# Performance work log

Hardware: AMD Instinct MI355X
Metric: run time of the kernel (lower is better)

The kernel has to match this reference:

```python
import jax, jax.numpy as jnp
import numpy as np

B, L, H = 2, 2048, 1024
NH, HD = 16, 64  # n_heads, head_size


def setup_inputs() -> dict:
    key = jax.random.key(0)
    ks = jax.random.split(key, 12)
    scale = 1.0 / np.sqrt(H)
    inp = {
        "hidden_states": jax.random.normal(ks[0], (B, L, H), dtype=jnp.float32),
        "tau": jax.random.uniform(ks[1], (B, 1), dtype=jnp.float32) + 0.5,
        "delta": jax.random.normal(ks[2], (B, L), dtype=jnp.float32) * 0.1,
        "Wq": jax.random.normal(ks[3], (H, H), dtype=jnp.float32) * scale,
        "bq": jnp.zeros((H,), dtype=jnp.float32),
        "Wk": jax.random.normal(ks[4], (H, H), dtype=jnp.float32) * scale,
        "bk": jnp.zeros((H,), dtype=jnp.float32),
        "Wv": jax.random.normal(ks[5], (H, H), dtype=jnp.float32) * scale,
        "bv": jnp.zeros((H,), dtype=jnp.float32),
        "Wo": jax.random.normal(ks[6], (H, H), dtype=jnp.float32) * scale,
        "bo": jnp.zeros((H,), dtype=jnp.float32),
    }
    return inp


def _split_heads(x):
    # [B, L, H] -> [B, NH, L, HD]
    return x.reshape(B, L, NH, HD).transpose(0, 2, 1, 3)


def reference(hidden_states, tau, delta, Wq, bq, Wk, bk, Wv, bv, Wo, bo):
    q = _split_heads(hidden_states @ Wq.T + bq)
    k = _split_heads(hidden_states @ Wk.T + bk)
    v = _split_heads(hidden_states @ Wv.T + bv)
    tau_b = tau[:, :, None, None]          # [B,1,1,1]
    delta_b = delta[:, None, None, :]      # [B,1,1,L]
    scores = jnp.einsum('bhqd,bhkd->bhqk', q, k) * tau_b + delta_b
    scores = scores / np.sqrt(HD)
    attn = jax.nn.softmax(scores, axis=-1)  # dropout = identity (eval mode)
    ctx = jnp.einsum('bhqk,bhkd->bhqd', attn, v)
    ctx = ctx.transpose(0, 2, 1, 3).reshape(B, L, H)
    return ctx @ Wo.T + bo
```

## Files before the change

kernel.cpp:

```cpp
#include <hip/hip_runtime.h>

#define B_ 2
#define L_ 2048
#define H_ 1024
#define NH_ 16
#define HD_ 64

using short8 = __attribute__((__ext_vector_type__(8))) short;
using f32x4 = __attribute__((__ext_vector_type__(4))) float;
using f32x16 = __attribute__((__ext_vector_type__(16))) float;
typedef unsigned short u16;
typedef unsigned int u32;

__device__ __forceinline__ u16 f2bf(float f) {
  union { float f; unsigned u; } x{f};
  unsigned u = x.u;
  u = u + 0x7FFFu + ((u >> 16) & 1u);
  return (u16)(u >> 16);
}

__device__ __forceinline__ void gld16(const void* g, void* l) {
  __builtin_amdgcn_global_load_lds(
      (const __attribute__((address_space(1))) void*)g,
      (__attribute__((address_space(3))) void*)l, 16, 0, 0);
}

#define MFMA16(a, b, c) __builtin_amdgcn_mfma_f32_16x16x32_bf16((a), (b), (c), 0, 0, 0)
#define MFMA32(a, b, c) __builtin_amdgcn_mfma_f32_32x32x16_bf16((a), (b), (c), 0, 0, 0)

__global__ void cast_all(const float* __restrict__ hs, const float* __restrict__ Wq,
                         const float* __restrict__ Wk, const float* __restrict__ Wv,
                         const float* __restrict__ Wo, const float* __restrict__ delta,
                         u16* __restrict__ dst, float* __restrict__ dsc) {
  const int t = blockIdx.x * 256 + threadIdx.x;
  const int i = t * 4;
  const float* src;
  int off;
  if (i < 4194304) {
    src = hs; off = i;
  } else {
    const int j = i - 4194304;
    const int w = j >> 20;
    off = j & 1048575;
    src = (w == 0) ? Wq : (w == 1) ? Wk : (w == 2) ? Wv : Wo;
  }
  float4 v = *(const float4*)(src + off);
  *(ushort4*)(dst + i) = make_ushort4(f2bf(v.x), f2bf(v.y), f2bf(v.z), f2bf(v.w));
  if (t < 4096) dsc[t] = delta[t] * 0.18033688011112042f;
}

__global__ __launch_bounds__(512) void gemm_qkv256(
    const u16* __restrict__ A, const u16* __restrict__ W,
    const float* __restrict__ bq, const float* __restrict__ bk, const float* __restrict__ bv,
    const float* __restrict__ tau,
    u16* __restrict__ qg, u16* __restrict__ kg, u16* __restrict__ vTg) {
  __shared__ u16 As[2][256 * 64];
  __shared__ u16 Bs[2][256 * 64];
  const int tid = threadIdx.x;
  const int lane = tid & 63;
  const int wid = tid >> 6;
  const int wr = wid >> 2;
  const int wc = wid & 3;
  const int orig = blockIdx.y * 12 + blockIdx.x;
  const int wg = (orig & 7) * 24 + (orig >> 3);
  const int m0 = (wg & 15) * 256;
  const int n0 = (wg >> 4) * 256;

  const int srow = tid >> 3;
  const int sg = tid & 7;

#define STAGE256(slot, t_)                                                              \
  {                                                                                     \
    const int kt64 = (t_) * 64;                                                         \
    _Pragma("unroll") for (int li = 0; li < 4; li++) {                                  \
      const int row = li * 64 + srow;                                                   \
      const int gsrc = sg ^ (row & 7);                                                  \
      gld16(A + (size_t)(m0 + row) * 1024 + kt64 + gsrc * 8,                            \
            (char*)As[slot] + li * 8192 + wid * 1024 + lane * 16);                      \
      gld16(W + (size_t)(n0 + row) * 1024 + kt64 + gsrc * 8,                            \
            (char*)Bs[slot] + li * 8192 + wid * 1024 + lane * 16);                      \
    }                                                                                   \
  }

  f32x4 acc[8][4] = {};

  STAGE256(0, 0);
  STAGE256(1, 1);

  for (int t = 0; t < 16; t++) {
    if (t >= 1 && t + 1 < 16) STAGE256((t + 1) & 1, t + 1);
    if (t + 1 < 16) {
      asm volatile("s_waitcnt vmcnt(8)" ::: "memory");
    } else {
      asm volatile("s_waitcnt vmcnt(0)" ::: "memory");
    }
    asm volatile("s_barrier" ::: "memory");
    const u16* Ab = As[t & 1];
    const u16* Bb = Bs[t & 1];
    short8 bf[4];
#pragma unroll
    for (int q = 0; q < 4; q++) {
      const int mh = q & 1, ks = q >> 1;
      const int g0 = ks * 4 + (lane >> 4);
      if (mh == 0) {
#pragma unroll
        for (int ni = 0; ni < 4; ni++) {
          const int r = wc * 64 + ni * 16 + (lane & 15);
          bf[ni] = *(const short8*)((const char*)Bb + r * 128 + ((g0 ^ (r & 7)) << 4));
        }
      }
      short8 af[4];
#pragma unroll
      for (int mi = 0; mi < 4; mi++) {
        const int r = wr * 128 + (mh * 4 + mi) * 16 + (lane & 15);
        af[mi] = *(const short8*)((const char*)Ab + r * 128 + ((g0 ^ (r & 7)) << 4));
      }
      __builtin_amdgcn_s_setprio(1);
#pragma unroll
      for (int mi = 0; mi < 4; mi++)
#pragma unroll
        for (int ni = 0; ni < 4; ni++)
          acc[mh * 4 + mi][ni] = MFMA16(af[mi], bf[ni], acc[mh * 4 + mi][ni]);
      __builtin_amdgcn_s_setprio(0);
      asm volatile("s_barrier" ::: "memory");
    }
  }

  const int which = n0 >> 10;
  const int b_blk = m0 >> 11;
  const float scl = (which == 0) ? tau[b_blk] * 0.18033688011112042f : 1.0f;
  const float* bias = which == 0 ? bq : (which == 1 ? bk : bv);
#pragma unroll
  for (int ni = 0; ni < 4; ni++) {
    const int n = n0 + wc * 64 + ni * 16 + (lane & 15);
    const int nn = n & 1023;
    const int h = nn >> 6, d = nn & 63;
    const float bb = bias[nn];
#pragma unroll
    for (int mi = 0; mi < 8; mi++) {
      const int mb = m0 + wr * 128 + mi * 16 + ((lane >> 4) << 2);
      const int b = mb >> 11;
      const int lq = mb & 2047;
      if (which == 2) {
        ushort4 pk = make_ushort4(f2bf(acc[mi][ni][0] + bb), f2bf(acc[mi][ni][1] + bb),
                                  f2bf(acc[mi][ni][2] + bb), f2bf(acc[mi][ni][3] + bb));
        *(ushort4*)&vTg[((size_t)(b * NH_ + h) * HD_ + d) * L_ + lq] = pk;
      } else {
        u16* dst = which == 0 ? qg : kg;
#pragma unroll
        for (int r = 0; r < 4; r++)
          dst[((size_t)(b * NH_ + h) * L_ + lq + r) * HD_ + d] = f2bf((acc[mi][ni][r] + bb) * scl);
      }
    }
  }
}

__global__ __launch_bounds__(512) void attn(
    const u16* __restrict__ qg, const u16* __restrict__ kg, const u16* __restrict__ vTg,
    const float* __restrict__ dsc, u16* __restrict__ ctxg) {
  __shared__ u16 lds[3][8192];
  const int tid = threadIdx.x;
  const int lane = tid & 63;
  const int wv = tid >> 6;
  const int lane31 = lane & 31;
  const int hi = lane >> 5;
  const int orig = blockIdx.x;
  const int wgid = (orig & 7) * 32 + (orig >> 3);
  const int bh = wgid >> 3;
  const int qblk = wgid & 7;
  const int b = bh >> 4;
  const int h = bh & 15;
  const int q0 = qblk * 256 + wv * 32;
  const u16* qb = qg + (size_t)bh * L_ * HD_;
  const u16* kb = kg + (size_t)bh * L_ * HD_;
  const u16* vb = vTg + (size_t)bh * HD_ * L_;
  const float* db = dsc + (size_t)b * L_;

  short8 qf[4];
#pragma unroll
  for (int ks = 0; ks < 4; ks++)
    qf[ks] = *(const short8*)&qb[(size_t)(q0 + lane31) * 64 + ks * 16 + hi * 8];

  union { u32 u[4]; short8 s; } onesu;
  const u32 ow = (lane31 == 0) ? 0x3F803F80u : 0u;
  onesu.u[0] = ow; onesu.u[1] = ow; onesu.u[2] = ow; onesu.u[3] = ow;
  const short8 onesf = onesu.s;

  f32x16 acc[2] = {};
  f32x16 accl = {};
  float mrun = -__builtin_inff();

#define STAGE(bp_, j0)                                                                    \
  {                                                                                       \
    u16* bp = (bp_);                                                                      \
    {                                                                                     \
      const int kt = wv >> 2, ks = wv & 3;                                                \
      gld16(kb + (size_t)((j0) + kt * 32 + lane31) * 64 + ks * 16 + hi * 8,               \
            bp + wv * 512 + lane * 8);                                                    \
    }                                                                                     \
    {                                                                                     \
      const int kt = wv >> 2, dt = (wv >> 1) & 1, ks2 = wv & 1;                           \
      gld16(vb + (size_t)(dt * 32 + lane31) * L_ + (j0) + kt * 32 + ks2 * 16 + hi * 8,    \
            bp + (8 + wv) * 512 + lane * 8);                                              \
    }                                                                                     \
  }

#define QK64(bp_, sA_, sB_)                                                               \
  {                                                                                       \
    const u16* bp = (bp_);                                                                \
    __builtin_amdgcn_s_setprio(1);                                                        \
    _Pragma("unroll") for (int ks = 0; ks < 4; ks++) {                                    \
      short8 kf0 = *(const short8*)&bp[(0 * 4 + ks) * 512 + lane * 8];                    \
      short8 kf1 = *(const short8*)&bp[(1 * 4 + ks) * 512 + lane * 8];                    \
      sA_ = MFMA32(kf0, qf[ks], sA_);                                                     \
      sB_ = MFMA32(kf1, qf[ks], sB_);                                                     \
    }                                                                                     \
    __builtin_amdgcn_s_setprio(0);                                                        \
  }

  STAGE(lds[0], 0);
  STAGE(lds[1], 64);
  __syncthreads();

  f32x16 sp0 = {}, sp1 = {};
  QK64(lds[0], sp0, sp1);

  int cur = 0, nxt = 1, fut = 2;
  for (int t = 0; t < 32; t++) {
    const int j0 = t * 64;
    if (t + 2 < 32) STAGE(lds[fut], j0 + 128);
    f32x16 sn0 = {}, sn1 = {};
    if (t + 1 < 32) QK64(lds[nxt], sn0, sn1);

#pragma unroll
    for (int g = 0; g < 4; g++) {
      float4 dl0 = *(const float4*)&db[j0 + g * 8 + hi * 4];
      float4 dl1 = *(const float4*)&db[j0 + 32 + g * 8 + hi * 4];
      sp0[g * 4 + 0] += dl0.x; sp0[g * 4 + 1] += dl0.y;
      sp0[g * 4 + 2] += dl0.z; sp0[g * 4 + 3] += dl0.w;
      sp1[g * 4 + 0] += dl1.x; sp1[g * 4 + 1] += dl1.y;
      sp1[g * 4 + 2] += dl1.z; sp1[g * 4 + 3] += dl1.w;
    }
    float tm[8];
#pragma unroll
    for (int r = 0; r < 8; r++) tm[r] = fmaxf(fmaxf(sp0[r], sp0[8 + r]), fmaxf(sp1[r], sp1[8 + r]));
#pragma unroll
    for (int r = 0; r < 4; r++) tm[r] = fmaxf(tm[r], tm[4 + r]);
    float pmax = fmaxf(fmaxf(tm[0], tm[1]), fmaxf(tm[2], tm[3]));
    pmax = fmaxf(pmax, __shfl_xor(pmax, 32));
    if (!__all(pmax - mrun <= 11.5f)) {
      float mnew = fmaxf(mrun, pmax);
      float al = __builtin_amdgcn_exp2f(mrun - mnew);
      mrun = mnew;
      accl[0] *= al;
#pragma unroll
      for (int dt = 0; dt < 2; dt++)
#pragma unroll
        for (int r = 0; r < 16; r++) acc[dt][r] *= al;
    }
#pragma unroll
    for (int r = 0; r < 16; r++) {
      sp0[r] = __builtin_amdgcn_exp2f(sp0[r] - mrun);
      sp1[r] = __builtin_amdgcn_exp2f(sp1[r] - mrun);
    }
    u32 pk[16];
#pragma unroll
    for (int i = 0; i < 8; i++) {
      asm("v_cvt_pk_bf16_f32 %0, %1, %2" : "=v"(pk[i]) : "v"(sp0[2 * i]), "v"(sp0[2 * i + 1]));
      asm("v_cvt_pk_bf16_f32 %0, %1, %2" : "=v"(pk[8 + i]) : "v"(sp1[2 * i]), "v"(sp1[2 * i + 1]));
    }
#pragma unroll
    for (int kt = 0; kt < 2; kt++) {
      asm volatile("v_permlane32_swap_b32 %0, %1" : "+v"(pk[kt * 8 + 0]), "+v"(pk[kt * 8 + 2]));
      asm volatile("v_permlane32_swap_b32 %0, %1" : "+v"(pk[kt * 8 + 1]), "+v"(pk[kt * 8 + 3]));
      asm volatile("v_permlane32_swap_b32 %0, %1" : "+v"(pk[kt * 8 + 4]), "+v"(pk[kt * 8 + 6]));
      asm volatile("v_permlane32_swap_b32 %0, %1" : "+v"(pk[kt * 8 + 5]), "+v"(pk[kt * 8 + 7]));
    }
    {
      const u16* bp = lds[cur];
      __builtin_amdgcn_s_setprio(1);
#pragma unroll
      for (int kt = 0; kt < 2; kt++)
#pragma unroll
        for (int ks2 = 0; ks2 < 2; ks2++) {
          union U8 { u32 u[4]; short8 s; } pf;
          pf.u[0] = pk[kt * 8 + ks2 * 4 + 0];
          pf.u[1] = pk[kt * 8 + ks2 * 4 + 1];
          pf.u[2] = pk[kt * 8 + ks2 * 4 + 2];
          pf.u[3] = pk[kt * 8 + ks2 * 4 + 3];
#pragma unroll
          for (int dt = 0; dt < 2; dt++) {
            short8 vf = *(const short8*)&bp[(8 + kt * 4 + dt * 2 + ks2) * 512 + lane * 8];
            acc[dt] = MFMA32(vf, pf.s, acc[dt]);
          }
          accl = MFMA32(onesf, pf.s, accl);
        }
      __builtin_amdgcn_s_setprio(0);
    }
    __syncthreads();
    sp0 = sn0; sp1 = sn1;
    const int tmp = cur; cur = nxt; nxt = fut; fut = tmp;
  }

  u16* tw = (u16*)lds + wv * 2048;
  const float l0 = accl[0];
  const float l1 = __shfl_xor(l0, 32);
  const float inv = 1.0f / (hi ? l1 : l0);
#pragma unroll
  for (int dt = 0; dt < 2; dt++)
#pragma unroll
    for (int g = 0; g < 4; g++) {
      ushort4 w4 = make_ushort4(f2bf(acc[dt][g * 4 + 0] * inv), f2bf(acc[dt][g * 4 + 1] * inv),
                                f2bf(acc[dt][g * 4 + 2] * inv), f2bf(acc[dt][g * 4 + 3] * inv));
      const int d0 = dt * 32 + g * 8 + hi * 4;
      const int byte = (lane31 * 128 + d0 * 2) ^ ((lane31 & 15) << 3);
      *(ushort4*)((char*)tw + byte) = w4;
    }
  asm volatile("s_waitcnt lgkmcnt(0)" ::: "memory");
  const size_t obase = ((size_t)b * L_ + q0) * 1024 + h * 64;
#pragma unroll
  for (int i = 0; i < 16; i++) {
    const int qr = 2 * i + hi;
    const int byte = (qr * 128 + lane31 * 4) ^ ((qr & 15) << 3);
    const u32 val = *(const u32*)((const char*)tw + byte);
    *(u32*)&ctxg[obase + (size_t)qr * 1024 + lane31 * 2] = val;
  }
}

__global__ __launch_bounds__(256) void gemm_out(
    const u16* __restrict__ A, const u16* __restrict__ W,
    const float* __restrict__ bo, float* __restrict__ out) {
  __shared__ u16 As[128 * 64];
  __shared__ u16 Bs[128 * 64];
  const int tid = threadIdx.x;
  const int lane = tid & 63;
  const int wave = tid >> 6;
  const int wrow = (wave >> 1) * 64;
  const int wcol = (wave & 1) * 64;
  const int m0 = blockIdx.y * 128;
  const int n0 = blockIdx.x * 128;
  const int rr = tid >> 3;
  const int c8 = (tid & 7) * 8;
  f32x4 acc[4][4] = {};
  for (int kt = 0; kt < 1024; kt += 64) {
#pragma unroll
    for (int i = 0; i < 4; i++) {
      gld16(A + (size_t)(m0 + i * 32 + rr) * 1024 + kt + c8, (char*)As + i * 4096 + wave * 1024);
      gld16(W + (size_t)(n0 + i * 32 + rr) * 1024 + kt + c8, (char*)Bs + i * 4096 + wave * 1024);
    }
    __syncthreads();
#pragma unroll
    for (int kc = 0; kc < 2; kc++) {
      const int ko = kc * 32 + (lane >> 4) * 8;
      short8 af[4], bf[4];
#pragma unroll
      for (int mi = 0; mi < 4; mi++)
        af[mi] = *(const short8*)&As[(wrow + mi * 16 + (lane & 15)) * 64 + ko];
#pragma unroll
      for (int ni = 0; ni < 4; ni++)
        bf[ni] = *(const short8*)&Bs[(wcol + ni * 16 + (lane & 15)) * 64 + ko];
#pragma unroll
      for (int mi = 0; mi < 4; mi++)
#pragma unroll
        for (int ni = 0; ni < 4; ni++)
          acc[mi][ni] = MFMA16(af[mi], bf[ni], acc[mi][ni]);
    }
    __syncthreads();
  }
#pragma unroll
  for (int ni = 0; ni < 4; ni++) {
    const int n = n0 + wcol + ni * 16 + (lane & 15);
    const float bb = bo[n];
#pragma unroll
    for (int mi = 0; mi < 4; mi++) {
      const int mb = m0 + wrow + mi * 16 + ((lane >> 4) << 2);
#pragma unroll
      for (int r = 0; r < 4; r++)
        out[(size_t)(mb + r) * 1024 + n] = acc[mi][ni][r] + bb;
    }
  }
}

extern "C" void kernel_launch(void* const* d_in, const int* in_sizes, int n_in,
                              void* d_out, int out_size, void* d_ws, size_t ws_size,
                              hipStream_t stream) {
  const float* hs = (const float*)d_in[0];
  const float* tau = (const float*)d_in[1];
  const float* delta = (const float*)d_in[2];
  const float* Wq = (const float*)d_in[3];
  const float* bq = (const float*)d_in[4];
  const float* Wk = (const float*)d_in[5];
  const float* bk = (const float*)d_in[6];
  const float* Wv = (const float*)d_in[7];
  const float* bv = (const float*)d_in[8];
  const float* Wo = (const float*)d_in[9];
  const float* bo = (const float*)d_in[10];
  float* out = (float*)d_out;

  u16* ws = (u16*)d_ws;
  u16* hsb  = ws;
  u16* wqkv = ws + 4194304;
  u16* wob  = ws + 7340032;
  u16* qg   = ws + 8388608;
  u16* kg   = ws + 12582912;
  u16* vTg  = ws + 16777216;
  u16* ctxg = ws + 20971520;
  float* dsc = (float*)(ws + 25165824);

  cast_all<<<8192, 256, 0, stream>>>(hs, Wq, Wk, Wv, Wo, delta, ws, dsc);

  gemm_qkv256<<<dim3(12, 16), 512, 0, stream>>>(hsb, wqkv, bq, bk, bv, tau, qg, kg, vTg);
  attn<<<256, 512, 0, stream>>>(qg, kg, vTg, dsc, ctxg);
  gemm_out<<<dim3(8, 32), 256, 0, stream>>>(ctxg, wob, bo, out);
}
```

Measured before the change: 147.1 us.

## Retile QKV GEMM to 256x192 and double-buffer the output GEMM

The QKV projection GEMM now uses 256x192 tiles, giving 256 workgroups instead of 192 so the grid covers the GPU's CUs in one wave. The epilogue picks q/k/v per 16-column subtile, since a tile can now straddle the q/k/v boundary. The output GEMM gains the same double-buffered, XOR-swizzled async LDS staging as the QKV kernel, plus grouped block ordering, in place of the single-buffered load-sync-compute loop. The cost is more LDS per block and a more complex epilogue. The B-tile width of 192 breaks the power-of-two layout assumptions.

```diff
diff --git a/kernel.cpp b/kernel.cpp
--- a/kernel.cpp
+++ b/kernel.cpp
@@ -49,27 +49,27 @@
   if (t < 4096) dsc[t] = delta[t] * 0.18033688011112042f;
 }
 
-__global__ __launch_bounds__(512) void gemm_qkv256(
+__global__ __launch_bounds__(512) void gemm_qkv192(
     const u16* __restrict__ A, const u16* __restrict__ W,
     const float* __restrict__ bq, const float* __restrict__ bk, const float* __restrict__ bv,
     const float* __restrict__ tau,
     u16* __restrict__ qg, u16* __restrict__ kg, u16* __restrict__ vTg) {
   __shared__ u16 As[2][256 * 64];
-  __shared__ u16 Bs[2][256 * 64];
+  __shared__ u16 Bs[2][192 * 64];
   const int tid = threadIdx.x;
   const int lane = tid & 63;
   const int wid = tid >> 6;
   const int wr = wid >> 2;
   const int wc = wid & 3;
-  const int orig = blockIdx.y * 12 + blockIdx.x;
-  const int wg = (orig & 7) * 24 + (orig >> 3);
+  const int orig = blockIdx.y * 16 + blockIdx.x;
+  const int wg = (orig & 7) * 32 + (orig >> 3);
   const int m0 = (wg & 15) * 256;
-  const int n0 = (wg >> 4) * 256;
+  const int n0 = (wg >> 4) * 192;
 
   const int srow = tid >> 3;
   const int sg = tid & 7;
 
-#define STAGE256(slot, t_)                                                              \
+#define STAGEQ(slot, t_)                                                                \
   {                                                                                     \
     const int kt64 = (t_) * 64;                                                         \
     _Pragma("unroll") for (int li = 0; li < 4; li++) {                                  \
@@ -77,35 +77,39 @@
       const int gsrc = sg ^ (row & 7);                                                  \
       gld16(A + (size_t)(m0 + row) * 1024 + kt64 + gsrc * 8,                            \
             (char*)As[slot] + li * 8192 + wid * 1024 + lane * 16);                      \
+    }                                                                                   \
+    _Pragma("unroll") for (int li = 0; li < 3; li++) {                                  \
+      const int row = li * 64 + srow;                                                   \
+      const int gsrc = sg ^ (row & 7);                                                  \
       gld16(W + (size_t)(n0 + row) * 1024 + kt64 + gsrc * 8,                            \
             (char*)Bs[slot] + li * 8192 + wid * 1024 + lane * 16);                      \
     }                                                                                   \
   }
 
-  f32x4 acc[8][4] = {};
-
-  STAGE256(0, 0);
-  STAGE256(1, 1);
+  f32x4 acc[8][3] = {};
+
+  STAGEQ(0, 0);
+  STAGEQ(1, 1);
 
   for (int t = 0; t < 16; t++) {
-    if (t >= 1 && t + 1 < 16) STAGE256((t + 1) & 1, t + 1);
+    if (t >= 1 && t + 1 < 16) STAGEQ((t + 1) & 1, t + 1);
     if (t + 1 < 16) {
-      asm volatile("s_waitcnt vmcnt(8)" ::: "memory");
+      asm volatile("s_waitcnt vmcnt(7)" ::: "memory");
     } else {
       asm volatile("s_waitcnt vmcnt(0)" ::: "memory");
     }
     asm volatile("s_barrier" ::: "memory");
     const u16* Ab = As[t & 1];
     const u16* Bb = Bs[t & 1];
-    short8 bf[4];
+    short8 bf[3];
 #pragma unroll
     for (int q = 0; q < 4; q++) {
       const int mh = q & 1, ks = q >> 1;
       const int g0 = ks * 4 + (lane >> 4);
       if (mh == 0) {
 #pragma unroll
-        for (int ni = 0; ni < 4; ni++) {
-          const int r = wc * 64 + ni * 16 + (lane & 15);
+        for (int ni = 0; ni < 3; ni++) {
+          const int r = wc * 48 + ni * 16 + (lane & 15);
           bf[ni] = *(const short8*)((const char*)Bb + r * 128 + ((g0 ^ (r & 7)) << 4));
         }
       }
@@ -119,23 +123,25 @@
 #pragma unroll
       for (int mi = 0; mi < 4; mi++)
 #pragma unroll
-        for (int ni = 0; ni < 4; ni++)
+        for (int ni = 0; ni < 3; ni++)
           acc[mh * 4 + mi][ni] = MFMA16(af[mi], bf[ni], acc[mh * 4 + mi][ni]);
       __builtin_amdgcn_s_setprio(0);
       asm volatile("s_barrier" ::: "memory");
     }
   }
 
-  const int which = n0 >> 10;
   const int b_blk = m0 >> 11;
-  const float scl = (which == 0) ? tau[b_blk] * 0.18033688011112042f : 1.0f;
-  const float* bias = which == 0 ? bq : (which == 1 ? bk : bv);
-#pragma unroll
-  for (int ni = 0; ni < 4; ni++) {
-    const int n = n0 + wc * 64 + ni * 16 + (lane & 15);
+  const float tauv = tau[b_blk] * 0.18033688011112042f;
+#pragma unroll
+  for (int ni = 0; ni < 3; ni++) {
+    const int nbase = n0 + wc * 48 + ni * 16;
+    const int which = nbase >> 10;
+    const int n = nbase + (lane & 15);
     const int nn = n & 1023;
     const int h = nn >> 6, d = nn & 63;
+    const float* bias = which == 0 ? bq : (which == 1 ? bk : bv);
     const float bb = bias[nn];
+    const float scl = which == 0 ? tauv : 1.0f;
 #pragma unroll
     for (int mi = 0; mi < 8; mi++) {
       const int mb = m0 + wr * 128 + mi * 16 + ((lane >> 4) << 2);
@@ -327,53 +333,88 @@
   }
 }
 
-__global__ __launch_bounds__(256) void gemm_out(
+__global__ __launch_bounds__(256) void gemm_out128(
     const u16* __restrict__ A, const u16* __restrict__ W,
     const float* __restrict__ bo, float* __restrict__ out) {
-  __shared__ u16 As[128 * 64];
-  __shared__ u16 Bs[128 * 64];
+  __shared__ u16 As[2][128 * 64];
+  __shared__ u16 Bs[2][128 * 64];
   const int tid = threadIdx.x;
   const int lane = tid & 63;
-  const int wave = tid >> 6;
-  const int wrow = (wave >> 1) * 64;
-  const int wcol = (wave & 1) * 64;
-  const int m0 = blockIdx.y * 128;
-  const int n0 = blockIdx.x * 128;
-  const int rr = tid >> 3;
-  const int c8 = (tid & 7) * 8;
+  const int wid = tid >> 6;
+  const int wr = wid >> 1;
+  const int wc = wid & 1;
+  const int orig = blockIdx.y * 8 + blockIdx.x;
+  const int wg = (orig & 7) * 32 + (orig >> 3);
+  const int m0 = (wg & 31) * 128;
+  const int n0 = (wg >> 5) * 128;
+
+  const int srow = tid >> 3;
+  const int sg = tid & 7;
+
+#define STAGEO(slot, t_)                                                                \
+  {                                                                                     \
+    const int kt64 = (t_) * 64;                                                         \
+    _Pragma("unroll") for (int li = 0; li < 4; li++) {                                  \
+      const int row = li * 32 + srow;                                                   \
+      const int gsrc = sg ^ (row & 7);                                                  \
+      gld16(A + (size_t)(m0 + row) * 1024 + kt64 + gsrc * 8,                            \
+            (char*)As[slot] + li * 4096 + wid * 1024 + lane * 16);                      \
+      gld16(W + (size_t)(n0 + row) * 1024 + kt64 + gsrc * 8,                            \
+            (char*)Bs[slot] + li * 4096 + wid * 1024 + lane * 16);                      \
+    }                                                                                   \
+  }
+
   f32x4 acc[4][4] = {};
-  for (int kt = 0; kt < 1024; kt += 64) {
-#pragma unroll
-    for (int i = 0; i < 4; i++) {
-      gld16(A + (size_t)(m0 + i * 32 + rr) * 1024 + kt + c8, (char*)As + i * 4096 + wave * 1024);
-      gld16(W + (size_t)(n0 + i * 32 + rr) * 1024 + kt + c8, (char*)Bs + i * 4096 + wave * 1024);
-    }
-    __syncthreads();
-#pragma unroll
-    for (int kc = 0; kc < 2; kc++) {
-      const int ko = kc * 32 + (lane >> 4) * 8;
-      short8 af[4], bf[4];
-#pragma unroll
-      for (int mi = 0; mi < 4; mi++)
-        af[mi] = *(const short8*)&As[(wrow + mi * 16 + (lane & 15)) * 64 + ko];
-#pragma unroll
-      for (int ni = 0; ni < 4; ni++)
-        bf[ni] = *(const short8*)&Bs[(wcol + ni * 16 + (lane & 15)) * 64 + ko];
-#pragma unroll
-      for (int mi = 0; mi < 4; mi++)
+
+  STAGEO(0, 0);
+  STAGEO(1, 1);
+
+  for (int t = 0; t < 16; t++) {
+    if (t >= 1 && t + 1 < 16) STAGEO((t + 1) & 1, t + 1);
+    if (t + 1 < 16) {
+      asm volatile("s_waitcnt vmcnt(8)" ::: "memory");
+    } else {
+      asm volatile("s_waitcnt vmcnt(0)" ::: "memory");
+    }
+    asm volatile("s_barrier" ::: "memory");
+    const u16* Ab = As[t & 1];
+    const u16* Bb = Bs[t & 1];
+    short8 bf[4];
+#pragma unroll
+    for (int q = 0; q < 4; q++) {
+      const int mh = q & 1, ks = q >> 1;
+      const int g0 = ks * 4 + (lane >> 4);
+      if (mh == 0) {
+#pragma unroll
+        for (int ni = 0; ni < 4; ni++) {
+          const int r = wc * 64 + ni * 16 + (lane & 15);
+          bf[ni] = *(const short8*)((const char*)Bb + r * 128 + ((g0 ^ (r & 7)) << 4));
+        }
+      }
+      short8 af[2];
+#pragma unroll
+      for (int mi = 0; mi < 2; mi++) {
+        const int r = wr * 64 + (mh * 2 + mi) * 16 + (lane & 15);
+        af[mi] = *(const short8*)((const char*)Ab + r * 128 + ((g0 ^ (r & 7)) << 4));
+      }
+      __builtin_amdgcn_s_setprio(1);
+#pragma unroll
+      for (int mi = 0; mi < 2; mi++)
 #pragma unroll
         for (int ni = 0; ni < 4; ni++)
-          acc[mi][ni] = MFMA16(af[mi], bf[ni], acc[mi][ni]);
-    }
-    __syncthreads();
-  }
+          acc[mh * 2 + mi][ni] = MFMA16(af[mi], bf[ni], acc[mh * 2 + mi][ni]);
+      __builtin_amdgcn_s_setprio(0);
+      asm volatile("s_barrier" ::: "memory");
+    }
+  }
+
 #pragma unroll
   for (int ni = 0; ni < 4; ni++) {
-    const int n = n0 + wcol + ni * 16 + (lane & 15);
+    const int n = n0 + wc * 64 + ni * 16 + (lane & 15);
     const float bb = bo[n];
 #pragma unroll
     for (int mi = 0; mi < 4; mi++) {
-      const int mb = m0 + wrow + mi * 16 + ((lane >> 4) << 2);
+      const int mb = m0 + wr * 64 + mi * 16 + ((lane >> 4) << 2);
 #pragma unroll
       for (int r = 0; r < 4; r++)
         out[(size_t)(mb + r) * 1024 + n] = acc[mi][ni][r] + bb;
@@ -409,7 +450,7 @@
 
   cast_all<<<8192, 256, 0, stream>>>(hs, Wq, Wk, Wv, Wo, delta, ws, dsc);
 
-  gemm_qkv256<<<dim3(12, 16), 512, 0, stream>>>(hsb, wqkv, bq, bk, bv, tau, qg, kg, vTg);
+  gemm_qkv192<<<dim3(16, 16), 512, 0, stream>>>(hsb, wqkv, bq, bk, bv, tau, qg, kg, vTg);
   attn<<<256, 512, 0, stream>>>(qg, kg, vTg, dsc, ctxg);
-  gemm_out<<<dim3(8, 32), 256, 0, stream>>>(ctxg, wob, bo, out);
-}
+  gemm_out128<<<dim3(8, 32), 256, 0, stream>>>(ctxg, wob, bo, out);
+}
```

Measured after the change: 139.2 us. -5.4%, faster.
